# Kernel tuning notes

Measured on AMD Instinct MI355X. Metric: run time of the kernel, lower is better.

The kernel has to match this reference:

```python
import jax, jax.numpy as jnp
import numpy as np

ETA = 3.0       # eta_px
KCAP = 96       # k_pos_cap
POS_W = 1.2     # obj_pos_weight
LCD = 1.0       # lambda_cd
LP0 = 1.0       # lambda_p0


def setup_inputs() -> dict:
    key = jax.random.key(0)
    k1, k2, k3, k4, k5, k6 = jax.random.split(key, 6)
    B, H, W, Ng, C = 4, 192, 192, 64, 4
    img = 192 * 8.0
    ctr = jax.random.uniform(k4, (B, Ng, 1, 2), minval=60.0, maxval=img - 60.0)
    offs = jax.random.normal(k5, (B, Ng, 3, 2)) * 30.0
    return {
        "pred_reg": jax.random.normal(k1, (B, 6, H, W), dtype=jnp.float32),
        "pred_obj": jax.random.normal(k2, (B, 1, H, W), dtype=jnp.float32),
        "pred_cls": jax.random.normal(k3, (B, C, H, W), dtype=jnp.float32),
        "gt_pts": (ctr + offs).astype(jnp.float32),
        "gt_lbl": jax.random.randint(k6, (B, Ng), 0, C),
        "stride": 8,
    }


def _loss_core(pred_reg, pred_obj, pred_cls, gt_pts, gt_lbl, stride):
    B, _, H, W = pred_reg.shape
    N = H * W
    C = pred_cls.shape[1]
    s = jnp.float32(stride)
    ys = (jnp.arange(H, dtype=jnp.float32) + 0.5) * s
    xs = (jnp.arange(W, dtype=jnp.float32) + 0.5) * s
    yy, xx = jnp.meshgrid(ys, xs, indexing='ij')
    px = xx.reshape(N)  # grid-center x, [N]
    py = yy.reshape(N)

    A = gt_pts[:, :, 0, :]   # [B,Ng,2]
    Bv = gt_pts[:, :, 1, :]
    Cv = gt_pts[:, :, 2, :]

    def sgn(P, Q):  # sign test of cell center vs edge (P,Q); broadcasts to [B,Ng,N]
        return (px - Q[..., 0:1]) * (P[..., 1:2] - Q[..., 1:2]) - (P[..., 0:1] - Q[..., 0:1]) * (py - Q[..., 1:2])

    d1 = sgn(A, Bv); d2 = sgn(Bv, Cv); d3 = sgn(Cv, A)
    has_neg = (d1 < 0) | (d2 < 0) | (d3 < 0)
    has_pos = (d1 > 0) | (d2 > 0) | (d3 > 0)
    inside = ~(has_neg & has_pos)  # [B,Ng,N]

    def seg(P, Q):  # point-to-segment distance, [B,Ng,N]
        vx = Q[..., 0:1] - P[..., 0:1]
        vy = Q[..., 1:2] - P[..., 1:2]
        wx = px - P[..., 0:1]
        wy = py - P[..., 1:2]
        t = jnp.clip((wx * vx + wy * vy) / (vx * vx + vy * vy + 1e-9), 0.0, 1.0)
        dx = wx - t * vx
        dy = wy - t * vy
        return jnp.sqrt(dx * dx + dy * dy + 1e-12)

    dist = jnp.minimum(seg(A, Bv), jnp.minimum(seg(Bv, Cv), seg(Cv, A)))  # [B,Ng,N]
    pos = inside | (dist <= ETA)

    # top-k cap: keep the KCAP closest positive cells per GT (matches torch topk(-d))
    dmask = jnp.where(pos, dist, jnp.inf)
    negv, idx = jax.lax.top_k(-dmask, KCAP)  # [B,Ng,KCAP]
    valid = jnp.isfinite(negv)               # True only for actual positives
    capped = jax.vmap(jax.vmap(lambda i, v: jnp.zeros((N,), bool).at[i].set(v)))(idx, valid)  # [B,Ng,N]

    # objectness BCE-with-logits with pos_weight, summed
    obj_t = capped.any(axis=1).astype(pred_obj.dtype)  # [B,N]
    x = pred_obj.reshape(B, N)
    obj_loss = jnp.sum(-(POS_W * obj_t * jax.nn.log_sigmoid(x) + (1.0 - obj_t) * jax.nn.log_sigmoid(-x)))

    # class targets: nearest GT (by triangle distance) among capped positives
    dcls = jnp.where(capped, dist, jnp.inf)
    jbest = jnp.argmin(dcls, axis=1)                   # [B,N]; first index on ties, like sequential strict <
    cellmask = jnp.isfinite(jnp.min(dcls, axis=1))     # [B,N]
    tgt = jnp.take_along_axis(gt_lbl, jbest, axis=1)   # [B,N]
    logits = pred_cls.reshape(B, C, N).transpose(0, 2, 1)  # [B,N,C]
    lse = jax.nn.logsumexp(logits, axis=-1)
    picked = jnp.take_along_axis(logits, tgt[..., None], axis=-1)[..., 0]
    cls_loss = jnp.sum(jnp.where(cellmask, lse - picked, 0.0))

    centers_flat = jnp.stack([px, py], axis=-1)        # [N,2]
    anchors = centers_flat[idx]                        # [B,Ng,K,2]
    pred_off = pred_reg.transpose(0, 2, 3, 1).reshape(B, N, 3, 2)
    pred_sel = jax.vmap(lambda p, i: p[i])(pred_off, idx)          # [B,Ng,K,3,2]
    gt_off = (gt_pts[:, :, None, :, :] - anchors[:, :, :, None, :]) / s  # [B,Ng,K,3,2]
    w = valid.astype(pred_reg.dtype)                   # [B,Ng,K]

    loss_p0 = jnp.sum(w * jnp.sum((pred_sel[..., 0, :] - gt_off[..., 0, :]) ** 2, axis=-1))
    # chamfer between the 2 tail points; original: chamfer_2pts(...) * npix == per-cell (d1+d2) summed
    dmat = jnp.sqrt(jnp.sum((pred_sel[:, :, :, 1:, None, :] - gt_off[:, :, :, None, 1:, :]) ** 2, axis=-1) + 1e-12)  # [B,Ng,K,2,2]
    cd = jnp.sum(w * (dmat.min(axis=-1).sum(axis=-1) + dmat.min(axis=-2).sum(axis=-1)))
    reg_loss = LP0 * loss_p0 + LCD * cd

    return jnp.stack([reg_loss, obj_loss, cls_loss])


def reference(pred_reg, pred_obj, pred_cls, gt_pts, gt_lbl, stride):
    return _loss_core(pred_reg, pred_obj, pred_cls, gt_pts, gt_lbl, stride)
```

## Files before the change

kernel.cpp:

```cpp
#include <hip/hip_runtime.h>
#include <stdint.h>

#define ETA    3.0f
#define KCAP   96
#define POS_W  1.2f
#define NG     64
#define BATCH  4
#define HH     192
#define WW     192
#define NCELL  (HH*WW)
#define NCLS   4
#define CAP    4096
#define PTHR   256
#define NWAVE  4
#define NBLK   (BATCH*NG)
#define NBB    128
#define LISTCAP (NBLK*KCAP)
#define TOPBIT 0x8000000000000000ull
#define INF64  0xFFFFFFFFFFFFFFFFull
#define FIXS   1048576.0f

#define WS_MEMSET_BYTES (16 + BATCH*NCELL*8)
#define WS_LIST_OFF     WS_MEMSET_BYTES
#define WS_PA_OFF       (WS_LIST_OFF + LISTCAP*4)

#define OBJ4_PER_BLK 144

__device__ __forceinline__ float log_sigmoid(float x) {
    return fminf(x, 0.0f) - __logf(1.0f + __expf(-fabsf(x)));
}

__device__ __forceinline__ float segsq(float wx, float wy, float vx, float vy, float inv) {
    float t = (wx * vx + wy * vy) * inv;
    t = fminf(fmaxf(t, 0.0f), 1.0f);
    float dx = wx - t * vx;
    float dy = wy - t * vy;
    return dx * dx + dy * dy;
}

__device__ __forceinline__ float block_sum(float v, float* buf) {
    #pragma unroll
    for (int off = 32; off > 0; off >>= 1) v += __shfl_down(v, off);
    const int lane = threadIdx.x & 63;
    const int wid  = threadIdx.x >> 6;
    __syncthreads();
    if (lane == 0) buf[wid] = v;
    __syncthreads();
    float r = 0.0f;
    if (threadIdx.x == 0) {
        #pragma unroll
        for (int w = 0; w < NWAVE; ++w) r += buf[w];
    }
    return r;
}

__global__ __launch_bounds__(PTHR)
void pair_kernel(const float* __restrict__ pred_reg,
                 const float* __restrict__ pred_obj,
                 const float* __restrict__ pred_cls,
                 const float* __restrict__ gt_pts,
                 const int*   __restrict__ stride_p,
                 unsigned long long* __restrict__ cellkey,
                 int* __restrict__ lcounter,
                 int* __restrict__ list,
                 float4* __restrict__ pA)
{
    const int pair = blockIdx.x;
    const int b    = pair >> 6;
    const int g    = pair & (NG - 1);
    const int tid  = threadIdx.x;
    const int lane = tid & 63;
    const int wid  = tid >> 6;
    const float s  = (float)(*stride_p);

    __shared__ unsigned long long keys[CAP];
    __shared__ int   hist[PTHR];
    __shared__ int   entries[KCAP];
    __shared__ float fbuf[NWAVE];
    __shared__ int   wsum[NWAVE];
    __shared__ int   scnt, lcnt, lbase, sd, sp;

    float c_obj = 0.0f;
    if (tid < OBJ4_PER_BLK) {
        const float4 v = ((const float4*)pred_obj)[pair * OBJ4_PER_BLK + tid];
        c_obj = -log_sigmoid(-v.x) - log_sigmoid(-v.y)
                - log_sigmoid(-v.z) - log_sigmoid(-v.w);
    }

    const float* gp = gt_pts + (size_t)pair * 6;
    const float Ax = gp[0], Ay = gp[1];
    const float Bx = gp[2], By = gp[3];
    const float Cx = gp[4], Cy = gp[5];

    const float vABx = Bx - Ax, vABy = By - Ay;
    const float vBCx = Cx - Bx, vBCy = Cy - By;
    const float vCAx = Ax - Cx, vCAy = Ay - Cy;
    const float invAB = 1.0f / (vABx * vABx + vABy * vABy + 1e-9f);
    const float invBC = 1.0f / (vBCx * vBCx + vBCy * vBCy + 1e-9f);
    const float invCA = 1.0f / (vCAx * vCAx + vCAy * vCAy + 1e-9f);

    const float xmin = fminf(Ax, fminf(Bx, Cx)) - ETA;
    const float xmax = fmaxf(Ax, fmaxf(Bx, Cx)) + ETA;
    const float ymin = fminf(Ay, fminf(By, Cy)) - ETA;
    const float ymax = fmaxf(Ay, fmaxf(By, Cy)) + ETA;
    const float inv_sf = 1.0f / s;
    int j0 = max(0,      (int)floorf(xmin * inv_sf - 0.5f) - 1);
    int j1 = min(WW - 1, (int)ceilf (xmax * inv_sf - 0.5f) + 1);
    int i0 = max(0,      (int)floorf(ymin * inv_sf - 0.5f) - 1);
    int i1 = min(HH - 1, (int)ceilf (ymax * inv_sf - 0.5f) + 1);
    const int nbw = j1 - j0 + 1;
    const int nbh = i1 - i0 + 1;
    const int nb  = (nbw > 0 && nbh > 0) ? nbw * nbh : 0;

    if (tid == 0) { scnt = 0; lcnt = 0; }
    __syncthreads();

    for (int t = tid; t < nb; t += PTHR) {
        const int li = t / nbw;
        const int lj = t - li * nbw;
        const int i = i0 + li;
        const int j = j0 + lj;
        const float px = ((float)j + 0.5f) * s;
        const float py = ((float)i + 0.5f) * s;

        const float d1 = (px - Bx) * (Ay - By) - (Ax - Bx) * (py - By);
        const float d2 = (px - Cx) * (By - Cy) - (Bx - Cx) * (py - Cy);
        const float d3 = (px - Ax) * (Cy - Ay) - (Cx - Ax) * (py - Ay);
        const bool has_neg = (d1 < 0.0f) | (d2 < 0.0f) | (d3 < 0.0f);
        const bool has_pos = (d1 > 0.0f) | (d2 > 0.0f) | (d3 > 0.0f);
        const bool inside = !(has_neg && has_pos);

        float dsq = segsq(px - Ax, py - Ay, vABx, vABy, invAB);
        dsq = fminf(dsq, segsq(px - Bx, py - By, vBCx, vBCy, invBC));
        dsq = fminf(dsq, segsq(px - Cx, py - Cy, vCAx, vCAy, invCA));
        const float dist = sqrtf(dsq + 1e-12f);

        if (inside || dist <= ETA) {
            int slot = atomicAdd(&scnt, 1);
            if (slot < CAP) {
                const int n = i * WW + j;
                keys[slot] = (((unsigned long long)__float_as_uint(dist)) << 16) | (unsigned)n;
            }
        }
    }
    __syncthreads();

    const int M = min(scnt, CAP);
    unsigned long long T = INF64;

    if (M > KCAP) {
        unsigned long long prefix = 0;
        int need = KCAP;
        for (int shift = 40; shift >= 0; shift -= 8) {
            hist[tid] = 0;
            __syncthreads();
            for (int t = tid; t < M; t += PTHR) {
                const unsigned long long k = keys[t];
                if ((k >> (shift + 8)) == prefix)
                    atomicAdd(&hist[(int)((k >> shift) & 0xFF)], 1);
            }
            __syncthreads();
            const int h = hist[tid];
            int incl = h;
            #pragma unroll
            for (int off = 1; off < 64; off <<= 1) {
                const int o = __shfl_up(incl, off);
                if (lane >= off) incl += o;
            }
            if (lane == 63) wsum[wid] = incl;
            __syncthreads();
            #pragma unroll
            for (int w = 0; w < NWAVE; ++w) if (w < wid) incl += wsum[w];
            const int excl = incl - h;
            if (excl < need && incl >= need) { sd = tid; sp = excl; }
            __syncthreads();
            prefix = (prefix << 8) | (unsigned)sd;
            need  -= sp;
            __syncthreads();
        }
        T = prefix;
    }

    float c_reg = 0.0f, c_lse = 0.0f;
    for (int t = tid; t < M; t += PTHR) {
        const unsigned long long k = keys[t];
        if (k > T) continue;
        const int   n    = (int)(k & 0xFFFFull);
        const float dist = __uint_as_float((unsigned)(k >> 16));
        const int   idx  = b * NCELL + n;

        const unsigned long long ck =
            (((unsigned long long)__float_as_uint(dist)) << 32) | (unsigned)g;
        const unsigned long long old = atomicMin(&cellkey[idx], ck);
        if (old >= TOPBIT) {
            const float x = pred_obj[idx];
            c_obj += (-POS_W * log_sigmoid(x)) + log_sigmoid(-x);
            const float* pc = pred_cls + (size_t)b * NCLS * NCELL + n;
            const float l0 = pc[0];
            const float l1 = pc[NCELL];
            const float l2 = pc[2 * NCELL];
            const float l3 = pc[3 * NCELL];
            const float m = fmaxf(fmaxf(l0, l1), fmaxf(l2, l3));
            c_lse += m + __logf(__expf(l0 - m) + __expf(l1 - m)
                              + __expf(l2 - m) + __expf(l3 - m));
            const int r = atomicAdd(&lcnt, 1);
            entries[r] = (b << 16) | n;
        }

        const int i = n / WW;
        const int j = n - i * WW;
        const float ax = ((float)j + 0.5f) * s;
        const float ay = ((float)i + 0.5f) * s;

        const float g0x = (Ax - ax) * inv_sf, g0y = (Ay - ay) * inv_sf;
        const float g1x = (Bx - ax) * inv_sf, g1y = (By - ay) * inv_sf;
        const float g2x = (Cx - ax) * inv_sf, g2y = (Cy - ay) * inv_sf;

        const float* pr = pred_reg + (size_t)b * 6 * NCELL + n;
        const float p0x = pr[0 * NCELL], p0y = pr[1 * NCELL];
        const float p1x = pr[2 * NCELL], p1y = pr[3 * NCELL];
        const float p2x = pr[4 * NCELL], p2y = pr[5 * NCELL];

        c_reg += (p0x - g0x) * (p0x - g0x) + (p0y - g0y) * (p0y - g0y);

        const float d11 = sqrtf((p1x - g1x) * (p1x - g1x) + (p1y - g1y) * (p1y - g1y) + 1e-12f);
        const float d12 = sqrtf((p1x - g2x) * (p1x - g2x) + (p1y - g2y) * (p1y - g2y) + 1e-12f);
        const float d21 = sqrtf((p2x - g1x) * (p2x - g1x) + (p2y - g1y) * (p2y - g1y) + 1e-12f);
        const float d22 = sqrtf((p2x - g2x) * (p2x - g2x) + (p2y - g2y) * (p2y - g2y) + 1e-12f);

        c_reg += fminf(d11, d12) + fminf(d21, d22)
               + fminf(d11, d21) + fminf(d12, d22);
    }
    __syncthreads();

    if (tid == 0) lbase = atomicAdd(lcounter, lcnt);
    __syncthreads();
    if (tid < lcnt) list[lbase + 1 + tid] = entries[tid];

    const float treg = block_sum(c_reg, fbuf);
    const float tobj = block_sum(c_obj, fbuf);
    const float tlse = block_sum(c_lse, fbuf);
    if (tid == 0) pA[pair] = make_float4(treg, tobj, tlse, 0.0f);
}

__global__ __launch_bounds__(PTHR)
void finish_kernel(const float* __restrict__ pred_cls,
                   const int*   __restrict__ gt_lbl,
                   const unsigned long long* __restrict__ cellkey,
                   const int*   __restrict__ lcounter,
                   const int*   __restrict__ list,
                   const float4* __restrict__ pA,
                   unsigned long long* __restrict__ fixacc,
                   int* __restrict__ arrival,
                   float* __restrict__ out)
{
    __shared__ float buf[NWAVE];
    __shared__ int islast;
    const int tid = threadIdx.x;
    const int count = *lcounter + 1;
    const int t = blockIdx.x * PTHR + tid;

    float c = 0.0f;
    if (t < count) {
        const int e = list[t];
        const int b = e >> 16;
        const int n = e & 0xFFFF;
        const unsigned long long k = cellkey[b * NCELL + n];
        const int g   = (int)(k & 0xFFFFFFFFull);
        const int tgt = gt_lbl[b * NG + g];
        c = -pred_cls[((size_t)(b * NCLS + tgt)) * NCELL + n];
    }
    const float sc = block_sum(c, buf);

    if (tid == 0) {
        islast = 0;
        const long long fx = (long long)(sc * FIXS);
        atomicAdd(fixacc, (unsigned long long)fx);
        __threadfence();
        const int old = atomicAdd(arrival, 1);
        if (old == NBB - 2) islast = 1;
    }
    __syncthreads();

    if (islast) {
        __threadfence();
        const float4 v = pA[tid];
        const float reg = block_sum(v.x, buf);
        const float obj = block_sum(v.y, buf);
        const float lse = block_sum(v.z, buf);
        if (tid == 0) {
            const unsigned long long tot = atomicAdd(fixacc, 0ull);
            const float picked = (float)((long long)tot + 1) * (1.0f / FIXS);
            out[0] = reg;
            out[1] = obj;
            out[2] = lse + picked;
        }
    }
}

extern "C" void kernel_launch(void* const* d_in, const int* in_sizes, int n_in,
                              void* d_out, int out_size, void* d_ws, size_t ws_size,
                              hipStream_t stream) {
    const float* pred_reg = (const float*)d_in[0];
    const float* pred_obj = (const float*)d_in[1];
    const float* pred_cls = (const float*)d_in[2];
    const float* gt_pts   = (const float*)d_in[3];
    const int*   gt_lbl   = (const int*)d_in[4];
    const int*   stride_p = (const int*)d_in[5];
    float* out = (float*)d_out;

    char* ws = (char*)d_ws;
    int* lcounter = (int*)ws;
    int* arrival  = (int*)(ws + 4);
    unsigned long long* fixacc = (unsigned long long*)(ws + 8);
    unsigned long long* cellkey = (unsigned long long*)(ws + 16);
    int*    list = (int*)(ws + WS_LIST_OFF);
    float4* pA   = (float4*)(ws + WS_PA_OFF);

    (void)in_sizes; (void)n_in; (void)ws_size; (void)out_size;

    hipMemsetAsync(ws, 0xFF, WS_MEMSET_BYTES, stream);
    hipLaunchKernelGGL(pair_kernel, dim3(NBLK), dim3(PTHR), 0, stream,
                       pred_reg, pred_obj, pred_cls, gt_pts, stride_p,
                       cellkey, lcounter, list, pA);
    hipLaunchKernelGGL(finish_kernel, dim3(NBB), dim3(PTHR), 0, stream,
                       pred_cls, gt_lbl, cellkey, lcounter, list, pA,
                       fixacc, arrival, out);
}
```

Before: 24.37 us.

## Fuse memset, pair and finish kernels into one cooperative kernel with grid syncs

Replaces the memset plus two-kernel pipeline with a single cooperative launch. Cell keys are initialised in-kernel, followed by a grid sync. The picked-class term is tracked incrementally through atomicMin winner transitions, using fixed-point deltas that subtract the displaced owner's logit and add the new one, which removes the entry list and the finish pass. A second grid sync lets block 0 reduce the per-block partials. This saves the launch and memset overhead, at the cost of two grid-wide barriers and a cooperative-launch requirement.

```diff
diff --git a/kernel.cpp b/kernel.cpp
--- a/kernel.cpp
+++ b/kernel.cpp
@@ -1,4 +1,5 @@
 #include <hip/hip_runtime.h>
+#include <hip/hip_cooperative_groups.h>
 #include <stdint.h>
 
 #define ETA    3.0f
@@ -14,17 +15,16 @@
 #define PTHR   256
 #define NWAVE  4
 #define NBLK   (BATCH*NG)
-#define NBB    128
-#define LISTCAP (NBLK*KCAP)
-#define TOPBIT 0x8000000000000000ull
 #define INF64  0xFFFFFFFFFFFFFFFFull
-#define FIXS   1048576.0f
-
-#define WS_MEMSET_BYTES (16 + BATCH*NCELL*8)
-#define WS_LIST_OFF     WS_MEMSET_BYTES
-#define WS_PA_OFF       (WS_LIST_OFF + LISTCAP*4)
+#define FIXS   67108864.0f
+#define INV_FIXS (1.0 / 67108864.0)
+
+#define WS_PA_OFF (BATCH*NCELL*8)
+#define WS_PB_OFF (WS_PA_OFF + NBLK*16)
 
 #define OBJ4_PER_BLK 144
+
+namespace cg = cooperative_groups;
 
 __device__ __forceinline__ float log_sigmoid(float x) {
     return fminf(x, 0.0f) - __logf(1.0f + __expf(-fabsf(x)));
@@ -38,33 +38,44 @@
     return dx * dx + dy * dy;
 }
 
-__device__ __forceinline__ float block_sum(float v, float* buf) {
+__device__ __forceinline__ void block_red(float a, float b, float c, long long f,
+                                          float* s3, long long* s1,
+                                          float out3[3], long long* outf) {
     #pragma unroll
-    for (int off = 32; off > 0; off >>= 1) v += __shfl_down(v, off);
+    for (int off = 32; off > 0; off >>= 1) {
+        a += __shfl_down(a, off);
+        b += __shfl_down(b, off);
+        c += __shfl_down(c, off);
+        f += __shfl_down(f, off);
+    }
     const int lane = threadIdx.x & 63;
     const int wid  = threadIdx.x >> 6;
     __syncthreads();
-    if (lane == 0) buf[wid] = v;
+    if (lane == 0) { s3[wid*3+0]=a; s3[wid*3+1]=b; s3[wid*3+2]=c; s1[wid]=f; }
     __syncthreads();
-    float r = 0.0f;
     if (threadIdx.x == 0) {
+        float ra=0.0f, rb=0.0f, rc=0.0f; long long rf=0;
         #pragma unroll
-        for (int w = 0; w < NWAVE; ++w) r += buf[w];
-    }
-    return r;
+        for (int w = 0; w < NWAVE; ++w) {
+            ra += s3[w*3+0]; rb += s3[w*3+1]; rc += s3[w*3+2]; rf += s1[w];
+        }
+        out3[0]=ra; out3[1]=rb; out3[2]=rc; *outf=rf;
+    }
 }
 
 __global__ __launch_bounds__(PTHR)
-void pair_kernel(const float* __restrict__ pred_reg,
-                 const float* __restrict__ pred_obj,
-                 const float* __restrict__ pred_cls,
-                 const float* __restrict__ gt_pts,
-                 const int*   __restrict__ stride_p,
-                 unsigned long long* __restrict__ cellkey,
-                 int* __restrict__ lcounter,
-                 int* __restrict__ list,
-                 float4* __restrict__ pA)
+void fused_kernel(const float* __restrict__ pred_reg,
+                  const float* __restrict__ pred_obj,
+                  const float* __restrict__ pred_cls,
+                  const float* __restrict__ gt_pts,
+                  const int*   __restrict__ gt_lbl,
+                  const int*   __restrict__ stride_p,
+                  unsigned long long* __restrict__ cellkey,
+                  float4* __restrict__ pA,
+                  long long* __restrict__ pB,
+                  float* __restrict__ out)
 {
+    cg::grid_group grid = cg::this_grid();
     const int pair = blockIdx.x;
     const int b    = pair >> 6;
     const int g    = pair & (NG - 1);
@@ -74,11 +85,14 @@
     const float s  = (float)(*stride_p);
 
     __shared__ unsigned long long keys[CAP];
-    __shared__ int   hist[PTHR];
-    __shared__ int   entries[KCAP];
-    __shared__ float fbuf[NWAVE];
-    __shared__ int   wsum[NWAVE];
-    __shared__ int   scnt, lcnt, lbase, sd, sp;
+    __shared__ int       hist[PTHR];
+    __shared__ float     s3[NWAVE*3];
+    __shared__ long long s1[NWAVE];
+    __shared__ int       wsum[NWAVE];
+    __shared__ int       scnt, sd, sp;
+
+    for (int i = pair * PTHR + tid; i < BATCH * NCELL; i += NBLK * PTHR)
+        cellkey[i] = INF64;
 
     float c_obj = 0.0f;
     if (tid < OBJ4_PER_BLK) {
@@ -86,6 +100,8 @@
         c_obj = -log_sigmoid(-v.x) - log_sigmoid(-v.y)
                 - log_sigmoid(-v.z) - log_sigmoid(-v.w);
     }
+
+    grid.sync();
 
     const float* gp = gt_pts + (size_t)pair * 6;
     const float Ax = gp[0], Ay = gp[1];
@@ -112,7 +128,7 @@
     const int nbh = i1 - i0 + 1;
     const int nb  = (nbw > 0 && nbh > 0) ? nbw * nbh : 0;
 
-    if (tid == 0) { scnt = 0; lcnt = 0; }
+    if (tid == 0) scnt = 0;
     __syncthreads();
 
     for (int t = tid; t < nb; t += PTHR) {
@@ -181,7 +197,11 @@
         T = prefix;
     }
 
+    const int tgt_mine = gt_lbl[pair];
+    const size_t bc = (size_t)b * NCLS * NCELL;
+
     float c_reg = 0.0f, c_lse = 0.0f;
+    long long fix = 0;
     for (int t = tid; t < M; t += PTHR) {
         const unsigned long long k = keys[t];
         if (k > T) continue;
@@ -192,19 +212,28 @@
         const unsigned long long ck =
             (((unsigned long long)__float_as_uint(dist)) << 32) | (unsigned)g;
         const unsigned long long old = atomicMin(&cellkey[idx], ck);
-        if (old >= TOPBIT) {
-            const float x = pred_obj[idx];
-            c_obj += (-POS_W * log_sigmoid(x)) + log_sigmoid(-x);
-            const float* pc = pred_cls + (size_t)b * NCLS * NCELL + n;
-            const float l0 = pc[0];
-            const float l1 = pc[NCELL];
-            const float l2 = pc[2 * NCELL];
-            const float l3 = pc[3 * NCELL];
-            const float m = fmaxf(fmaxf(l0, l1), fmaxf(l2, l3));
-            c_lse += m + __logf(__expf(l0 - m) + __expf(l1 - m)
-                              + __expf(l2 - m) + __expf(l3 - m));
-            const int r = atomicAdd(&lcnt, 1);
-            entries[r] = (b << 16) | n;
+        if (old > ck) {
+            const float* pc = pred_cls + bc + n;
+            if (old == INF64) {
+                const float x = pred_obj[idx];
+                c_obj += (-POS_W * log_sigmoid(x)) + log_sigmoid(-x);
+                const float l0 = pc[0];
+                const float l1 = pc[NCELL];
+                const float l2 = pc[2 * NCELL];
+                const float l3 = pc[3 * NCELL];
+                const float m = fmaxf(fmaxf(l0, l1), fmaxf(l2, l3));
+                c_lse += m + __logf(__expf(l0 - m) + __expf(l1 - m)
+                                  + __expf(l2 - m) + __expf(l3 - m));
+                const float pm = (tgt_mine == 0) ? l0 :
+                                 (tgt_mine == 1) ? l1 :
+                                 (tgt_mine == 2) ? l2 : l3;
+                fix -= __float2ll_rn(pm * FIXS);
+            } else {
+                const int gold = (int)(old & 0xFFFFFFFFull);
+                const int tgto = gt_lbl[b * NG + gold];
+                fix -= __float2ll_rn(pc[(size_t)tgt_mine * NCELL] * FIXS);
+                fix += __float2ll_rn(pc[(size_t)tgto     * NCELL] * FIXS);
+            }
         }
 
         const int i = n / WW;
@@ -231,69 +260,24 @@
         c_reg += fminf(d11, d12) + fminf(d21, d22)
                + fminf(d11, d21) + fminf(d12, d22);
     }
-    __syncthreads();
-
-    if (tid == 0) lbase = atomicAdd(lcounter, lcnt);
-    __syncthreads();
-    if (tid < lcnt) list[lbase + 1 + tid] = entries[tid];
-
-    const float treg = block_sum(c_reg, fbuf);
-    const float tobj = block_sum(c_obj, fbuf);
-    const float tlse = block_sum(c_lse, fbuf);
-    if (tid == 0) pA[pair] = make_float4(treg, tobj, tlse, 0.0f);
-}
-
-__global__ __launch_bounds__(PTHR)
-void finish_kernel(const float* __restrict__ pred_cls,
-                   const int*   __restrict__ gt_lbl,
-                   const unsigned long long* __restrict__ cellkey,
-                   const int*   __restrict__ lcounter,
-                   const int*   __restrict__ list,
-                   const float4* __restrict__ pA,
-                   unsigned long long* __restrict__ fixacc,
-                   int* __restrict__ arrival,
-                   float* __restrict__ out)
-{
-    __shared__ float buf[NWAVE];
-    __shared__ int islast;
-    const int tid = threadIdx.x;
-    const int count = *lcounter + 1;
-    const int t = blockIdx.x * PTHR + tid;
-
-    float c = 0.0f;
-    if (t < count) {
-        const int e = list[t];
-        const int b = e >> 16;
-        const int n = e & 0xFFFF;
-        const unsigned long long k = cellkey[b * NCELL + n];
-        const int g   = (int)(k & 0xFFFFFFFFull);
-        const int tgt = gt_lbl[b * NG + g];
-        c = -pred_cls[((size_t)(b * NCLS + tgt)) * NCELL + n];
-    }
-    const float sc = block_sum(c, buf);
-
+
+    float out3[3]; long long ftot;
+    block_red(c_reg, c_obj, c_lse, fix, s3, s1, out3, &ftot);
     if (tid == 0) {
-        islast = 0;
-        const long long fx = (long long)(sc * FIXS);
-        atomicAdd(fixacc, (unsigned long long)fx);
-        __threadfence();
-        const int old = atomicAdd(arrival, 1);
-        if (old == NBB - 2) islast = 1;
-    }
-    __syncthreads();
-
-    if (islast) {
-        __threadfence();
-        const float4 v = pA[tid];
-        const float reg = block_sum(v.x, buf);
-        const float obj = block_sum(v.y, buf);
-        const float lse = block_sum(v.z, buf);
+        pA[pair] = make_float4(out3[0], out3[1], out3[2], 0.0f);
+        pB[pair] = ftot;
+    }
+
+    grid.sync();
+
+    if (pair == 0) {
+        const float4    v = pA[tid];
+        const long long f = pB[tid];
+        block_red(v.x, v.y, v.z, f, s3, s1, out3, &ftot);
         if (tid == 0) {
-            const unsigned long long tot = atomicAdd(fixacc, 0ull);
-            const float picked = (float)((long long)tot + 1) * (1.0f / FIXS);
-            out[0] = reg;
-            out[1] = obj;
-            out[2] = lse + picked;
+            out[0] = out3[0];
+            out[1] = out3[1];
+            out[2] = out3[2] + (float)((double)ftot * INV_FIXS);
         }
     }
 }
@@ -310,20 +294,14 @@
     float* out = (float*)d_out;
 
     char* ws = (char*)d_ws;
-    int* lcounter = (int*)ws;
-    int* arrival  = (int*)(ws + 4);
-    unsigned long long* fixacc = (unsigned long long*)(ws + 8);
-    unsigned long long* cellkey = (unsigned long long*)(ws + 16);
-    int*    list = (int*)(ws + WS_LIST_OFF);
-    float4* pA   = (float4*)(ws + WS_PA_OFF);
+    unsigned long long* cellkey = (unsigned long long*)ws;
+    float4*    pA = (float4*)(ws + WS_PA_OFF);
+    long long* pB = (long long*)(ws + WS_PB_OFF);
 
     (void)in_sizes; (void)n_in; (void)ws_size; (void)out_size;
 
-    hipMemsetAsync(ws, 0xFF, WS_MEMSET_BYTES, stream);
-    hipLaunchKernelGGL(pair_kernel, dim3(NBLK), dim3(PTHR), 0, stream,
-                       pred_reg, pred_obj, pred_cls, gt_pts, stride_p,
-                       cellkey, lcounter, list, pA);
-    hipLaunchKernelGGL(finish_kernel, dim3(NBB), dim3(PTHR), 0, stream,
-                       pred_cls, gt_lbl, cellkey, lcounter, list, pA,
-                       fixacc, arrival, out);
-}
+    void* args[] = { &pred_reg, &pred_obj, &pred_cls, &gt_pts, &gt_lbl, &stride_p,
+                     &cellkey, &pA, &pB, &out };
+    hipLaunchCooperativeKernel(reinterpret_cast<void*>(fused_kernel),
+                               dim3(NBLK), dim3(PTHR), args, 0, stream);
+}
```

Result: slower. 68.26 us (+180.1%).

## Replace global cellkey atomics and memset with per-pair claim lists resolved in shared memory

Applied to the files above, without the earlier changes.

Removes the 1.2MB memset of a global per-cell key array and the global atomicMin arbitration. Each pair block now writes its up-to-KCAP claimed cells to a compact list. A second kernel, one block per batch segment, resolves ownership with shared-memory atomicMin tables and computes the obj, lse and picked-class terms. It also replaces the fixed-point global accumulation with per-block partials summed by the last-arriving block, and fuses the block reductions. The cost is that every resolve block scans all claims of its batch.

```diff
diff --git a/kernel.cpp b/kernel.cpp
--- a/kernel.cpp
+++ b/kernel.cpp
@@ -14,15 +14,17 @@
 #define PTHR   256
 #define NWAVE  4
 #define NBLK   (BATCH*NG)
-#define NBB    128
-#define LISTCAP (NBLK*KCAP)
+#define SEGS   16
+#define NB2    (BATCH*SEGS)
+#define SEGC   (NCELL/SEGS)
+#define BCLAIM (NG*KCAP)
+#define INF64  0xFFFFFFFFFFFFFFFFull
 #define TOPBIT 0x8000000000000000ull
-#define INF64  0xFFFFFFFFFFFFFFFFull
-#define FIXS   1048576.0f
-
-#define WS_MEMSET_BYTES (16 + BATCH*NCELL*8)
-#define WS_LIST_OFF     WS_MEMSET_BYTES
-#define WS_PA_OFF       (WS_LIST_OFF + LISTCAP*4)
+
+#define WS_CCNT_OFF   16
+#define WS_CLAIM_OFF  (WS_CCNT_OFF + NBLK*4)
+#define WS_PA_OFF     (WS_CLAIM_OFF + NBLK*KCAP*8)
+#define WS_PC_OFF     (WS_PA_OFF + NBLK*16)
 
 #define OBJ4_PER_BLK 144
 
@@ -38,36 +40,43 @@
     return dx * dx + dy * dy;
 }
 
-__device__ __forceinline__ float block_sum(float v, float* buf) {
+__device__ __forceinline__ void block_red5(float v[5], float* sbuf) {
     #pragma unroll
-    for (int off = 32; off > 0; off >>= 1) v += __shfl_down(v, off);
+    for (int off = 32; off > 0; off >>= 1) {
+        #pragma unroll
+        for (int q = 0; q < 5; ++q) v[q] += __shfl_down(v[q], off);
+    }
     const int lane = threadIdx.x & 63;
     const int wid  = threadIdx.x >> 6;
     __syncthreads();
-    if (lane == 0) buf[wid] = v;
-    __syncthreads();
-    float r = 0.0f;
+    if (lane == 0) {
+        #pragma unroll
+        for (int q = 0; q < 5; ++q) sbuf[wid * 5 + q] = v[q];
+    }
+    __syncthreads();
     if (threadIdx.x == 0) {
         #pragma unroll
-        for (int w = 0; w < NWAVE; ++w) r += buf[w];
-    }
-    return r;
+        for (int q = 0; q < 5; ++q) {
+            float r = 0.0f;
+            #pragma unroll
+            for (int w = 0; w < NWAVE; ++w) r += sbuf[w * 5 + q];
+            v[q] = r;
+        }
+    }
 }
 
 __global__ __launch_bounds__(PTHR)
 void pair_kernel(const float* __restrict__ pred_reg,
                  const float* __restrict__ pred_obj,
-                 const float* __restrict__ pred_cls,
                  const float* __restrict__ gt_pts,
                  const int*   __restrict__ stride_p,
-                 unsigned long long* __restrict__ cellkey,
-                 int* __restrict__ lcounter,
-                 int* __restrict__ list,
-                 float4* __restrict__ pA)
+                 int* __restrict__ ccnt,
+                 unsigned long long* __restrict__ claims,
+                 float4* __restrict__ pA,
+                 int* __restrict__ arrival)
 {
     const int pair = blockIdx.x;
     const int b    = pair >> 6;
-    const int g    = pair & (NG - 1);
     const int tid  = threadIdx.x;
     const int lane = tid & 63;
     const int wid  = tid >> 6;
@@ -75,10 +84,11 @@
 
     __shared__ unsigned long long keys[CAP];
     __shared__ int   hist[PTHR];
-    __shared__ int   entries[KCAP];
-    __shared__ float fbuf[NWAVE];
+    __shared__ float sbuf[NWAVE * 5];
     __shared__ int   wsum[NWAVE];
-    __shared__ int   scnt, lcnt, lbase, sd, sp;
+    __shared__ int   scnt, ccl, sd, sp;
+
+    if (pair == 0 && tid == 0) *arrival = 0;
 
     float c_obj = 0.0f;
     if (tid < OBJ4_PER_BLK) {
@@ -112,7 +122,7 @@
     const int nbh = i1 - i0 + 1;
     const int nb  = (nbw > 0 && nbh > 0) ? nbw * nbh : 0;
 
-    if (tid == 0) { scnt = 0; lcnt = 0; }
+    if (tid == 0) { scnt = 0; ccl = 0; }
     __syncthreads();
 
     for (int t = tid; t < nb; t += PTHR) {
@@ -181,31 +191,16 @@
         T = prefix;
     }
 
-    float c_reg = 0.0f, c_lse = 0.0f;
+    float c_reg = 0.0f;
     for (int t = tid; t < M; t += PTHR) {
         const unsigned long long k = keys[t];
         if (k > T) continue;
-        const int   n    = (int)(k & 0xFFFFull);
-        const float dist = __uint_as_float((unsigned)(k >> 16));
-        const int   idx  = b * NCELL + n;
-
-        const unsigned long long ck =
-            (((unsigned long long)__float_as_uint(dist)) << 32) | (unsigned)g;
-        const unsigned long long old = atomicMin(&cellkey[idx], ck);
-        if (old >= TOPBIT) {
-            const float x = pred_obj[idx];
-            c_obj += (-POS_W * log_sigmoid(x)) + log_sigmoid(-x);
-            const float* pc = pred_cls + (size_t)b * NCLS * NCELL + n;
-            const float l0 = pc[0];
-            const float l1 = pc[NCELL];
-            const float l2 = pc[2 * NCELL];
-            const float l3 = pc[3 * NCELL];
-            const float m = fmaxf(fmaxf(l0, l1), fmaxf(l2, l3));
-            c_lse += m + __logf(__expf(l0 - m) + __expf(l1 - m)
-                              + __expf(l2 - m) + __expf(l3 - m));
-            const int r = atomicAdd(&lcnt, 1);
-            entries[r] = (b << 16) | n;
-        }
+        const int n = (int)(k & 0xFFFFull);
+
+        const int slot = atomicAdd(&ccl, 1);
+        if (slot < KCAP)
+            claims[(size_t)pair * KCAP + slot] =
+                ((k >> 16) << 32) | (unsigned long long)(unsigned)n;
 
         const int i = n / WW;
         const int j = n - i * WW;
@@ -232,69 +227,116 @@
                + fminf(d11, d21) + fminf(d12, d22);
     }
     __syncthreads();
-
-    if (tid == 0) lbase = atomicAdd(lcounter, lcnt);
-    __syncthreads();
-    if (tid < lcnt) list[lbase + 1 + tid] = entries[tid];
-
-    const float treg = block_sum(c_reg, fbuf);
-    const float tobj = block_sum(c_obj, fbuf);
-    const float tlse = block_sum(c_lse, fbuf);
-    if (tid == 0) pA[pair] = make_float4(treg, tobj, tlse, 0.0f);
+    if (tid == 0) ccnt[pair] = min(ccl, KCAP);
+
+    float v[5] = { c_reg, c_obj, 0.0f, 0.0f, 0.0f };
+    block_red5(v, sbuf);
+    if (tid == 0) pA[pair] = make_float4(v[0], v[1], 0.0f, 0.0f);
 }
 
 __global__ __launch_bounds__(PTHR)
-void finish_kernel(const float* __restrict__ pred_cls,
-                   const int*   __restrict__ gt_lbl,
-                   const unsigned long long* __restrict__ cellkey,
-                   const int*   __restrict__ lcounter,
-                   const int*   __restrict__ list,
-                   const float4* __restrict__ pA,
-                   unsigned long long* __restrict__ fixacc,
-                   int* __restrict__ arrival,
-                   float* __restrict__ out)
+void resolve_kernel(const float* __restrict__ pred_obj,
+                    const float* __restrict__ pred_cls,
+                    const int*   __restrict__ gt_lbl,
+                    const int*   __restrict__ ccnt,
+                    const unsigned long long* __restrict__ claims,
+                    const float4* __restrict__ pA,
+                    float4* __restrict__ pC,
+                    int* __restrict__ arrival,
+                    float* __restrict__ out)
 {
-    __shared__ float buf[NWAVE];
-    __shared__ int islast;
+    const int blk = blockIdx.x;
+    const int b   = blk >> 4;
+    const int seg = blk & (SEGS - 1);
+    const int n0  = seg * SEGC;
     const int tid = threadIdx.x;
-    const int count = *lcounter + 1;
-    const int t = blockIdx.x * PTHR + tid;
-
-    float c = 0.0f;
-    if (t < count) {
-        const int e = list[t];
-        const int b = e >> 16;
-        const int n = e & 0xFFFF;
-        const unsigned long long k = cellkey[b * NCELL + n];
-        const int g   = (int)(k & 0xFFFFFFFFull);
+
+    __shared__ unsigned int       table[SEGC];
+    __shared__ unsigned long long cl[BCLAIM];
+    __shared__ int   cnts[NG];
+    __shared__ float sbuf[NWAVE * 5];
+    __shared__ int   ccl, islast;
+
+    if (tid < NG) cnts[tid] = ccnt[b * NG + tid];
+    if (tid == 0) { ccl = 0; islast = 0; }
+    for (int i = tid; i < SEGC; i += PTHR) table[i] = 0xFFFFFFFFu;
+    __syncthreads();
+
+    const unsigned long long* bcl = claims + (size_t)b * BCLAIM;
+    for (int sIdx = tid; sIdx < BCLAIM; sIdx += PTHR) {
+        const int pg = sIdx / KCAP;
+        const int r  = sIdx - pg * KCAP;
+        if (r < cnts[pg]) {
+            const unsigned long long e = bcl[sIdx];
+            const int ln = (int)(e & 0xFFFFull) - n0;
+            if ((unsigned)ln < (unsigned)SEGC) {
+                const int i = atomicAdd(&ccl, 1);
+                cl[i] = e | ((unsigned long long)pg << 16);
+                atomicMin(&table[ln], (unsigned)(e >> 32));
+            }
+        }
+    }
+    __syncthreads();
+    const int NC = ccl;
+
+    for (int i = tid; i < NC; i += PTHR) {
+        const unsigned long long e = cl[i];
+        const int ln = (int)(e & 0xFFFFull) - n0;
+        if (table[ln] == (unsigned)(e >> 32)) cl[i] = e | TOPBIT;
+    }
+    __syncthreads();
+    for (int i = tid; i < NC; i += PTHR) {
+        const unsigned long long e = cl[i];
+        if (e & TOPBIT) {
+            const int ln = (int)(e & 0xFFFFull) - n0;
+            atomicMin(&table[ln], (unsigned)((e >> 16) & 63ull));
+        }
+    }
+    __syncthreads();
+
+    float v[5] = { 0.0f, 0.0f, 0.0f, 0.0f, 0.0f };
+    const size_t bc = (size_t)b * NCLS * NCELL;
+    for (int i = tid; i < NC; i += PTHR) {
+        const unsigned long long e = cl[i];
+        if (!(e & TOPBIT)) continue;
+        const int n = (int)(e & 0xFFFFull);
+        const int g = (int)((e >> 16) & 63ull);
+        if (table[n - n0] != (unsigned)g) continue;
+
+        const float x = pred_obj[b * NCELL + n];
+        v[0] += (-POS_W * log_sigmoid(x)) + log_sigmoid(-x);
+
+        const float* pc = pred_cls + bc + n;
+        const float l0 = pc[0];
+        const float l1 = pc[NCELL];
+        const float l2 = pc[2 * NCELL];
+        const float l3 = pc[3 * NCELL];
+        const float m = fmaxf(fmaxf(l0, l1), fmaxf(l2, l3));
+        v[1] += m + __logf(__expf(l0 - m) + __expf(l1 - m)
+                         + __expf(l2 - m) + __expf(l3 - m));
         const int tgt = gt_lbl[b * NG + g];
-        c = -pred_cls[((size_t)(b * NCLS + tgt)) * NCELL + n];
-    }
-    const float sc = block_sum(c, buf);
+        v[2] += (tgt == 0) ? l0 : (tgt == 1) ? l1 : (tgt == 2) ? l2 : l3;
+    }
+    block_red5(v, sbuf);
 
     if (tid == 0) {
-        islast = 0;
-        const long long fx = (long long)(sc * FIXS);
-        atomicAdd(fixacc, (unsigned long long)fx);
+        pC[blk] = make_float4(v[0], v[1], v[2], 0.0f);
         __threadfence();
         const int old = atomicAdd(arrival, 1);
-        if (old == NBB - 2) islast = 1;
-    }
-    __syncthreads();
-
-    if (islast) {
-        __threadfence();
-        const float4 v = pA[tid];
-        const float reg = block_sum(v.x, buf);
-        const float obj = block_sum(v.y, buf);
-        const float lse = block_sum(v.z, buf);
-        if (tid == 0) {
-            const unsigned long long tot = atomicAdd(fixacc, 0ull);
-            const float picked = (float)((long long)tot + 1) * (1.0f / FIXS);
-            out[0] = reg;
-            out[1] = obj;
-            out[2] = lse + picked;
-        }
+        if (old == NB2 - 1) islast = 1;
+    }
+    __syncthreads();
+    if (!islast) return;
+    __threadfence();
+
+    const float4 a = pA[tid];
+    const float4 c = (tid < NB2) ? pC[tid] : make_float4(0.f, 0.f, 0.f, 0.f);
+    float w[5] = { a.x, a.y, c.x, c.y, c.z };
+    block_red5(w, sbuf);
+    if (tid == 0) {
+        out[0] = w[0];
+        out[1] = w[1] + w[2];
+        out[2] = w[3] - w[4];
     }
 }
 
@@ -310,20 +352,18 @@
     float* out = (float*)d_out;
 
     char* ws = (char*)d_ws;
-    int* lcounter = (int*)ws;
-    int* arrival  = (int*)(ws + 4);
-    unsigned long long* fixacc = (unsigned long long*)(ws + 8);
-    unsigned long long* cellkey = (unsigned long long*)(ws + 16);
-    int*    list = (int*)(ws + WS_LIST_OFF);
-    float4* pA   = (float4*)(ws + WS_PA_OFF);
+    int* arrival = (int*)ws;
+    int* ccnt    = (int*)(ws + WS_CCNT_OFF);
+    unsigned long long* claims = (unsigned long long*)(ws + WS_CLAIM_OFF);
+    float4* pA = (float4*)(ws + WS_PA_OFF);
+    float4* pC = (float4*)(ws + WS_PC_OFF);
 
     (void)in_sizes; (void)n_in; (void)ws_size; (void)out_size;
 
-    hipMemsetAsync(ws, 0xFF, WS_MEMSET_BYTES, stream);
     hipLaunchKernelGGL(pair_kernel, dim3(NBLK), dim3(PTHR), 0, stream,
-                       pred_reg, pred_obj, pred_cls, gt_pts, stride_p,
-                       cellkey, lcounter, list, pA);
-    hipLaunchKernelGGL(finish_kernel, dim3(NBB), dim3(PTHR), 0, stream,
-                       pred_cls, gt_lbl, cellkey, lcounter, list, pA,
-                       fixacc, arrival, out);
-}
+                       pred_reg, pred_obj, gt_pts, stride_p,
+                       ccnt, claims, pA, arrival);
+    hipLaunchKernelGGL(resolve_kernel, dim3(NB2), dim3(PTHR), 0, stream,
+                       pred_obj, pred_cls, gt_lbl, ccnt, claims, pA,
+                       pC, arrival, out);
+}
```

Measured after the change: 22.25 us. -8.7%, faster.
